# Kernel tuning notes

Measured on AMD Instinct MI355X. Metric: run time of the kernel, lower is better.

Reference implementation:

```python
import jax, jax.numpy as jnp
import numpy as np

MARGIN = 1.0
N, D, NUM_CLASSES = 8192, 512, 64


def setup_inputs() -> dict:
    key = jax.random.key(0)
    kz, kl = jax.random.split(key)
    z = jax.random.normal(kz, (N, D), dtype=jnp.float32)
    labels = jax.random.randint(kl, (N,), 0, NUM_CLASSES, dtype=jnp.int64)
    return {"z": z, "labels": labels}


def _pairwise_dist(z):
    # ||zi - zj|| via gram trick; zero-safe sqrt (grad 0 at zero distance, like torch.cdist)
    sq = jnp.sum(z * z, axis=1)  # [N]
    d2 = jnp.maximum(sq[:, None] + sq[None, :] - 2.0 * (z @ z.T), 0.0)  # [N, N]
    safe = d2 > 0
    return jnp.where(safe, jnp.sqrt(jnp.where(safe, d2, 1.0)), 0.0)


def reference(z, labels):
    n = z.shape[0]
    dist = _pairwise_dist(z)                       # [N, N]
    same = labels[:, None] == labels[None, :]      # [N, N] bool (includes self)
    pos_cnt = jnp.sum(same, axis=1)                # [N] >= 1 (self)
    neg_cnt = n - pos_cnt
    pos_mean = jnp.sum(jnp.where(same, dist, 0.0), axis=1) / jnp.maximum(pos_cnt, 1)
    neg_mean = jnp.sum(jnp.where(same, 0.0, dist), axis=1) / jnp.maximum(neg_cnt, 1)
    valid = (pos_cnt > 1) & (neg_cnt > 0)
    per_row = jax.nn.relu(pos_mean - neg_mean + MARGIN)
    total = jnp.sum(jnp.where(valid, per_row, 0.0))
    count = jnp.sum(valid)
    return total / jnp.maximum(count, 1)
```

## Files before the change

kernel.cpp:

```cpp
#include <hip/hip_runtime.h>
#include <hip/hip_bf16.h>
#include <hip/hip_fp8.h>
#include <stdint.h>

#define NROW 8192
#define DIM  512
#define BM   128
#define BN   128
#define BKB  128
#define NTK  (DIM / BKB)
#define NT   (NROW / BM)
#define NBLK (NT * (NT + 1) / 2)

typedef float f32x4 __attribute__((ext_vector_type(4)));
typedef int   i32x4 __attribute__((ext_vector_type(4)));
typedef int   i32x8 __attribute__((ext_vector_type(8)));

__device__ __forceinline__ float fast_sqrtf(float x) {
    return __builtin_amdgcn_sqrtf(x);
}

__device__ __forceinline__ unsigned char f32_to_e4m3(float f) {
    __hip_fp8_e4m3 q(f);
    return (unsigned char)q.__x;
}

__global__ __launch_bounds__(256) void prep_kernel(
    const float* __restrict__ z, const int* __restrict__ labels,
    unsigned char* __restrict__ zq, float* __restrict__ sq,
    int* __restrict__ hist, float* __restrict__ totals,
    int* __restrict__ done_ctr)
{
    if (blockIdx.x == NROW / 4) {
        __shared__ int lh[64];
        const int tid = threadIdx.x;
        if (tid < 64) lh[tid] = 0;
        __syncthreads();
        for (int i = tid; i < NROW; i += 256)
            atomicAdd(&lh[labels[i]], 1);
        __syncthreads();
        if (tid < 64) hist[tid] = lh[tid];
        if (tid == 64) { totals[0] = 0.f; totals[1] = 0.f; }
        if (tid == 65) { *done_ctr = 0; }
        return;
    }

    const int lane = threadIdx.x & 63;
    const int wave = threadIdx.x >> 6;
    const int row  = blockIdx.x * 4 + wave;

    const float4* zr = (const float4*)(z + (size_t)row * DIM);
    float4 v0 = zr[lane * 2 + 0];
    float4 v1 = zr[lane * 2 + 1];
    float s = v0.x*v0.x + v0.y*v0.y + v0.z*v0.z + v0.w*v0.w
            + v1.x*v1.x + v1.y*v1.y + v1.z*v1.z + v1.w*v1.w;

    union { unsigned char b[8]; int2 v; } pk;
    pk.b[0] = f32_to_e4m3(v0.x); pk.b[1] = f32_to_e4m3(v0.y);
    pk.b[2] = f32_to_e4m3(v0.z); pk.b[3] = f32_to_e4m3(v0.w);
    pk.b[4] = f32_to_e4m3(v1.x); pk.b[5] = f32_to_e4m3(v1.y);
    pk.b[6] = f32_to_e4m3(v1.z); pk.b[7] = f32_to_e4m3(v1.w);
    ((int2*)(zq + (size_t)row * DIM))[lane] = pk.v;

    #pragma unroll
    for (int sft = 1; sft < 64; sft <<= 1) s += __shfl_xor(s, sft);
    if (lane == 0) sq[row] = s;
}

__global__ __launch_bounds__(256, 3) void tile_kernel(
    const unsigned char* __restrict__ zq,
    const float* __restrict__ sq, const int* __restrict__ labels,
    float* __restrict__ partial_pos, float* __restrict__ partial_neg)
{
    __shared__ unsigned char As[BM * BKB];
    __shared__ unsigned char Bs[BN * BKB];

    const int tid  = threadIdx.x;
    const int lane = tid & 63;
    const int wave = tid >> 6;
    const int wm = wave >> 1;
    const int wn = wave & 1;

    const int bid  = (int)blockIdx.x;
    int bidx = (bid & 7) * (NBLK / 8) + (bid >> 3);
    int tm = 0, rem = bidx;
    while (rem >= NT - tm) { rem -= NT - tm; ++tm; }
    const int tn = tm + rem;
    const int row0 = tm * BM;
    const int col0 = tn * BN;
    const bool offdiag = (tm != tn);

    f32x4 acc[4][4];
    #pragma unroll
    for (int m = 0; m < 4; ++m)
        #pragma unroll
        for (int n = 0; n < 4; ++n)
            acc[m][n] = (f32x4){0.f, 0.f, 0.f, 0.f};

    const int srow   = tid >> 3;
    const int sinner = (tid & 7) << 4;
    const int kbsw   = sinner ^ ((srow & 7) << 4);
    const unsigned char* baseA = zq + (size_t)(row0 + srow) * DIM + kbsw;
    const unsigned char* baseB = zq + (size_t)(col0 + srow) * DIM + kbsw;

    const int swz  = (lane & 7) << 4;
    const int hi32 = (lane >> 4) << 5;
    const unsigned char* apc0 = As + (wm * 64 + (lane & 15)) * BKB + ((hi32 +  0) ^ swz);
    const unsigned char* apc1 = As + (wm * 64 + (lane & 15)) * BKB + ((hi32 + 16) ^ swz);
    const unsigned char* bpc0 = Bs + (wn * 64 + (lane & 15)) * BKB + ((hi32 +  0) ^ swz);
    const unsigned char* bpc1 = Bs + (wn * 64 + (lane & 15)) * BKB + ((hi32 + 16) ^ swz);

#define FRAG(pc0, pc1, off)                                                    \
    __builtin_shufflevector(*(const i32x4*)((pc0) + (off)),                    \
                            *(const i32x4*)((pc1) + (off)), 0, 1, 2, 3, 4, 5, 6, 7)

#define MFMA128(a, b, c)                                                       \
    __builtin_amdgcn_mfma_scale_f32_16x16x128_f8f6f4(                          \
        (a), (b), (c), 0, 0, 0, 0x7F7F7F7F, 0, 0x7F7F7F7F)

    #pragma unroll 1
    for (int t = 0; t < NTK; ++t) {
        const int k0 = t * BKB;
        #pragma unroll
        for (int r = 0; r < 4; ++r) {
            __builtin_amdgcn_global_load_lds(
                (const __attribute__((address_space(1))) void*)(baseA + (size_t)r * 32 * DIM + k0),
                (__attribute__((address_space(3))) void*)(As + r * 4096 + tid * 16),
                16, 0, 0);
            __builtin_amdgcn_global_load_lds(
                (const __attribute__((address_space(1))) void*)(baseB + (size_t)r * 32 * DIM + k0),
                (__attribute__((address_space(3))) void*)(Bs + r * 4096 + tid * 16),
                16, 0, 0);
        }
        __syncthreads();

        i32x8 bg0 = FRAG(bpc0, bpc1, 0 * 2048);
        i32x8 bg1 = FRAG(bpc0, bpc1, 1 * 2048);
        i32x8 bg2 = FRAG(bpc0, bpc1, 2 * 2048);
        i32x8 bg3 = FRAG(bpc0, bpc1, 3 * 2048);
        #pragma unroll
        for (int m = 0; m < 4; ++m) {
            i32x8 af = FRAG(apc0, apc1, m * 2048);
            acc[m][0] = MFMA128(af, bg0, acc[m][0]);
            acc[m][1] = MFMA128(af, bg1, acc[m][1]);
            acc[m][2] = MFMA128(af, bg2, acc[m][2]);
            acc[m][3] = MFMA128(af, bg3, acc[m][3]);
        }
        __syncthreads();
    }
#undef FRAG
#undef MFMA128

    const int colbase = col0 + wn * 64;
    const int hi = lane >> 4;
    float csq[4]; int clb[4];
    #pragma unroll
    for (int n = 0; n < 4; ++n) {
        int cg = colbase + n * 16 + (lane & 15);
        csq[n] = sq[cg];
        clb[n] = labels[cg];
    }
    float cpos[4] = {0.f, 0.f, 0.f, 0.f};
    float cneg[4] = {0.f, 0.f, 0.f, 0.f};

    float* rp = (float*)As;
    float* rn = rp + 256;
    float* cp = rp + 512;
    float* cn = rp + 768;

    #pragma unroll
    for (int m = 0; m < 4; ++m) {
        #pragma unroll
        for (int r = 0; r < 4; ++r) {
            const int rowl = wm * 64 + m * 16 + hi * 4 + r;
            const int rg = row0 + rowl;
            const float rs = sq[rg];
            const int   rl = labels[rg];
            float pos = 0.f, neg = 0.f;
            #pragma unroll
            for (int n = 0; n < 4; ++n) {
                float d2   = rs + csq[n] - 2.0f * acc[m][n][r];
                float dist = d2 > 0.f ? fast_sqrtf(d2) : 0.f;
                int cg = colbase + n * 16 + (lane & 15);
                if (cg == rg) dist = 0.f;
                bool same = (rl == clb[n]);
                float dp = same ? dist : 0.f;
                float dn = same ? 0.f : dist;
                pos += dp;  neg += dn;
                cpos[n] += dp;  cneg[n] += dn;
            }
            #pragma unroll
            for (int s = 1; s < 16; s <<= 1) {
                pos += __shfl_xor(pos, s);
                neg += __shfl_xor(neg, s);
            }
            if ((lane & 15) == 0) {
                rp[wn * 128 + rowl] = pos;
                rn[wn * 128 + rowl] = neg;
            }
        }
    }

    #pragma unroll
    for (int n = 0; n < 4; ++n) {
        cpos[n] += __shfl_xor(cpos[n], 16);
        cpos[n] += __shfl_xor(cpos[n], 32);
        cneg[n] += __shfl_xor(cneg[n], 16);
        cneg[n] += __shfl_xor(cneg[n], 32);
        if (lane < 16) {
            int coll = wn * 64 + n * 16 + lane;
            cp[wm * 128 + coll] = cpos[n];
            cn[wm * 128 + coll] = cneg[n];
        }
    }
    __syncthreads();

    if (tid < 128) {
        float p  = rp[tid] + rp[128 + tid];
        float nn = rn[tid] + rn[128 + tid];
        partial_pos[(size_t)tn * NROW + row0 + tid] = p;
        partial_neg[(size_t)tn * NROW + row0 + tid] = nn;
        if (offdiag) {
            float p2 = cp[tid] + cp[128 + tid];
            float n2 = cn[tid] + cn[128 + tid];
            partial_pos[(size_t)tm * NROW + col0 + tid] = p2;
            partial_neg[(size_t)tm * NROW + col0 + tid] = n2;
        }
    }
}

__global__ __launch_bounds__(256) void rowloss_kernel(
    const float* __restrict__ partial_pos, const float* __restrict__ partial_neg,
    const int* __restrict__ labels, const int* __restrict__ hist,
    float* __restrict__ totals, int* __restrict__ done_ctr,
    float* __restrict__ out)
{
    const int i = blockIdx.x * 256 + threadIdx.x;
    float ps = 0.f, ns = 0.f;
    #pragma unroll 8
    for (int s = 0; s < NT; ++s) {
        ps += partial_pos[(size_t)s * NROW + i];
        ns += partial_neg[(size_t)s * NROW + i];
    }
    const float pc = (float)hist[labels[i]];
    const float nc = (float)NROW - pc;
    const float pm = ps / fmaxf(pc, 1.f);
    const float nm = ns / fmaxf(nc, 1.f);
    const bool valid = (pc > 1.f) && (nc > 0.f);
    float t = valid ? fmaxf(pm - nm + 1.0f, 0.f) : 0.f;
    float c = valid ? 1.f : 0.f;
    #pragma unroll
    for (int s = 1; s < 64; s <<= 1) {
        t += __shfl_xor(t, s);
        c += __shfl_xor(c, s);
    }
    __shared__ float blk[8];
    const int wv = threadIdx.x >> 6;
    if ((threadIdx.x & 63) == 0) { blk[wv] = t; blk[4 + wv] = c; }
    __syncthreads();
    if (threadIdx.x == 0) {
        atomicAdd(&totals[0], blk[0] + blk[1] + blk[2] + blk[3]);
        atomicAdd(&totals[1], blk[4] + blk[5] + blk[6] + blk[7]);
        __threadfence();
        int prev = atomicAdd(done_ctr, 1);
        if (prev == (int)gridDim.x - 1) {
            float tt = atomicAdd(&totals[0], 0.f);
            float cc = atomicAdd(&totals[1], 0.f);
            out[0] = tt / fmaxf(cc, 1.f);
        }
    }
}

extern "C" void kernel_launch(void* const* d_in, const int* in_sizes, int n_in,
                              void* d_out, int out_size, void* d_ws, size_t ws_size,
                              hipStream_t stream) {
    (void)in_sizes; (void)n_in; (void)out_size; (void)ws_size;
    const float* z      = (const float*)d_in[0];
    const int*   labels = (const int*)d_in[1];
    float*       out    = (float*)d_out;

    char* ws = (char*)d_ws;
    float* partial_pos = (float*)(ws);
    float* partial_neg = (float*)(ws + 2097152);
    int*   hist     = (int*)  (ws + 4194304);
    float* totals   = (float*)(ws + 4194560);
    int*   done_ctr = (int*)  (ws + 4194568);
    unsigned char* zq = (unsigned char*)(ws + 4194816);
    float* sq       = (float*)(ws + 4194816 + (size_t)NROW * DIM);

    prep_kernel    <<<NROW / 4 + 1, 256, 0, stream>>>(z, labels, zq, sq, hist,
                                                      totals, done_ctr);
    tile_kernel    <<<NBLK, 256, 0, stream>>>(zq, sq, labels, partial_pos, partial_neg);
    rowloss_kernel <<<NROW / 256, 256, 0, stream>>>(partial_pos, partial_neg, labels,
                                                    hist, totals, done_ctr, out);
}
```

Baseline: 65.06 us.

## Double-buffer LDS tiles and split tile kernel across eight waves

The tile kernel now uses 512 threads, so each of eight waves computes a 32x64 sub-tile instead of 64x64. LDS is double-buffered so the next K-slice's global-to-LDS loads are issued before the current slice's MFMAs, leaving one barrier per iteration. The column-partial reduction in the epilogue now sums four wave-row contributions. Shared memory per block doubles to 64KB, which limits how many blocks fit on a CU. With only four K iterations, the overlap has little room to pay off.

After: 152.8 us. +134.8%, slower.

```diff
diff --git a/kernel.cpp b/kernel.cpp
--- a/kernel.cpp
+++ b/kernel.cpp
@@ -67,13 +67,13 @@
     if (lane == 0) sq[row] = s;
 }
 
-__global__ __launch_bounds__(256, 3) void tile_kernel(
+__global__ __launch_bounds__(512, 4) void tile_kernel(
     const unsigned char* __restrict__ zq,
     const float* __restrict__ sq, const int* __restrict__ labels,
     float* __restrict__ partial_pos, float* __restrict__ partial_neg)
 {
-    __shared__ unsigned char As[BM * BKB];
-    __shared__ unsigned char Bs[BN * BKB];
+    __shared__ unsigned char As[2 * BM * BKB];
+    __shared__ unsigned char Bs[2 * BN * BKB];
 
     const int tid  = threadIdx.x;
     const int lane = tid & 63;
@@ -90,9 +90,9 @@
     const int col0 = tn * BN;
     const bool offdiag = (tm != tn);
 
-    f32x4 acc[4][4];
-    #pragma unroll
-    for (int m = 0; m < 4; ++m)
+    f32x4 acc[2][4];
+    #pragma unroll
+    for (int m = 0; m < 2; ++m)
         #pragma unroll
         for (int n = 0; n < 4; ++n)
             acc[m][n] = (f32x4){0.f, 0.f, 0.f, 0.f};
@@ -105,42 +105,44 @@
 
     const int swz  = (lane & 7) << 4;
     const int hi32 = (lane >> 4) << 5;
-    const unsigned char* apc0 = As + (wm * 64 + (lane & 15)) * BKB + ((hi32 +  0) ^ swz);
-    const unsigned char* apc1 = As + (wm * 64 + (lane & 15)) * BKB + ((hi32 + 16) ^ swz);
+    const unsigned char* apc0 = As + (wm * 32 + (lane & 15)) * BKB + ((hi32 +  0) ^ swz);
+    const unsigned char* apc1 = As + (wm * 32 + (lane & 15)) * BKB + ((hi32 + 16) ^ swz);
     const unsigned char* bpc0 = Bs + (wn * 64 + (lane & 15)) * BKB + ((hi32 +  0) ^ swz);
     const unsigned char* bpc1 = Bs + (wn * 64 + (lane & 15)) * BKB + ((hi32 + 16) ^ swz);
 
 #define FRAG(pc0, pc1, off)                                                    \
     __builtin_shufflevector(*(const i32x4*)((pc0) + (off)),                    \
                             *(const i32x4*)((pc1) + (off)), 0, 1, 2, 3, 4, 5, 6, 7)
-
 #define MFMA128(a, b, c)                                                       \
     __builtin_amdgcn_mfma_scale_f32_16x16x128_f8f6f4(                          \
         (a), (b), (c), 0, 0, 0, 0x7F7F7F7F, 0, 0x7F7F7F7F)
-
-    #pragma unroll 1
+#define STAGE(bufofs, k0)                                                      \
+    do {                                                                       \
+        _Pragma("unroll")                                                      \
+        for (int r = 0; r < 2; ++r) {                                          \
+            __builtin_amdgcn_global_load_lds(                                  \
+                (const __attribute__((address_space(1))) void*)(baseA + (size_t)r * 64 * DIM + (k0)), \
+                (__attribute__((address_space(3))) void*)(As + (bufofs) + r * 8192 + tid * 16), 16, 0, 0); \
+            __builtin_amdgcn_global_load_lds(                                  \
+                (const __attribute__((address_space(1))) void*)(baseB + (size_t)r * 64 * DIM + (k0)), \
+                (__attribute__((address_space(3))) void*)(Bs + (bufofs) + r * 8192 + tid * 16), 16, 0, 0); \
+        }                                                                      \
+    } while (0)
+
+    STAGE(0, 0);
+    __syncthreads();
+    #pragma unroll
     for (int t = 0; t < NTK; ++t) {
-        const int k0 = t * BKB;
+        const int cur = (t & 1) * 16384;
+        const int nxt = ((t + 1) & 1) * 16384;
+        if (t + 1 < NTK) STAGE(nxt, (t + 1) * BKB);
+        i32x8 bg0 = FRAG(bpc0 + cur, bpc1 + cur, 0 * 2048);
+        i32x8 bg1 = FRAG(bpc0 + cur, bpc1 + cur, 1 * 2048);
+        i32x8 bg2 = FRAG(bpc0 + cur, bpc1 + cur, 2 * 2048);
+        i32x8 bg3 = FRAG(bpc0 + cur, bpc1 + cur, 3 * 2048);
         #pragma unroll
-        for (int r = 0; r < 4; ++r) {
-            __builtin_amdgcn_global_load_lds(
-                (const __attribute__((address_space(1))) void*)(baseA + (size_t)r * 32 * DIM + k0),
-                (__attribute__((address_space(3))) void*)(As + r * 4096 + tid * 16),
-                16, 0, 0);
-            __builtin_amdgcn_global_load_lds(
-                (const __attribute__((address_space(1))) void*)(baseB + (size_t)r * 32 * DIM + k0),
-                (__attribute__((address_space(3))) void*)(Bs + r * 4096 + tid * 16),
-                16, 0, 0);
-        }
-        __syncthreads();
-
-        i32x8 bg0 = FRAG(bpc0, bpc1, 0 * 2048);
-        i32x8 bg1 = FRAG(bpc0, bpc1, 1 * 2048);
-        i32x8 bg2 = FRAG(bpc0, bpc1, 2 * 2048);
-        i32x8 bg3 = FRAG(bpc0, bpc1, 3 * 2048);
-        #pragma unroll
-        for (int m = 0; m < 4; ++m) {
-            i32x8 af = FRAG(apc0, apc1, m * 2048);
+        for (int m = 0; m < 2; ++m) {
+            i32x8 af = FRAG(apc0 + cur, apc1 + cur, m * 2048);
             acc[m][0] = MFMA128(af, bg0, acc[m][0]);
             acc[m][1] = MFMA128(af, bg1, acc[m][1]);
             acc[m][2] = MFMA128(af, bg2, acc[m][2]);
@@ -150,6 +152,7 @@
     }
 #undef FRAG
 #undef MFMA128
+#undef STAGE
 
     const int colbase = col0 + wn * 64;
     const int hi = lane >> 4;
@@ -166,13 +169,13 @@
     float* rp = (float*)As;
     float* rn = rp + 256;
     float* cp = rp + 512;
-    float* cn = rp + 768;
-
-    #pragma unroll
-    for (int m = 0; m < 4; ++m) {
+    float* cn = rp + 1024;
+
+    #pragma unroll
+    for (int m = 0; m < 2; ++m) {
         #pragma unroll
         for (int r = 0; r < 4; ++r) {
-            const int rowl = wm * 64 + m * 16 + hi * 4 + r;
+            const int rowl = wm * 32 + m * 16 + hi * 4 + r;
             const int rg = row0 + rowl;
             const float rs = sq[rg];
             const int   rl = labels[rg];
@@ -221,8 +224,8 @@
         partial_pos[(size_t)tn * NROW + row0 + tid] = p;
         partial_neg[(size_t)tn * NROW + row0 + tid] = nn;
         if (offdiag) {
-            float p2 = cp[tid] + cp[128 + tid];
-            float n2 = cn[tid] + cn[128 + tid];
+            float p2 = cp[tid] + cp[128 + tid] + cp[256 + tid] + cp[384 + tid];
+            float n2 = cn[tid] + cn[128 + tid] + cn[256 + tid] + cn[384 + tid];
             partial_pos[(size_t)tm * NROW + col0 + tid] = p2;
             partial_neg[(size_t)tm * NROW + col0 + tid] = n2;
         }
@@ -290,7 +293,7 @@
 
     prep_kernel    <<<NROW / 4 + 1, 256, 0, stream>>>(z, labels, zq, sq, hist,
                                                       totals, done_ctr);
-    tile_kernel    <<<NBLK, 256, 0, stream>>>(zq, sq, labels, partial_pos, partial_neg);
+    tile_kernel    <<<NBLK, 512, 0, stream>>>(zq, sq, labels, partial_pos, partial_neg);
     rowloss_kernel <<<NROW / 256, 256, 0, stream>>>(partial_pos, partial_neg, labels,
                                                     hist, totals, done_ctr, out);
 }
```

## Replace row shuffle reductions with LDS transpose and track total instead of negative

Applied to the files above, without the earlier changes.

The epilogue now accumulates pos and total distance and derives neg as total minus pos, which removes a select per element. Per-row partials are written to a padded LDS buffer, and 128 threads then sum them with vector loads, replacing the 16-lane shuffle reductions. The diagonal check is precomputed per lane as a predicate. Shared memory grows to about 42KB, which may reduce occupancy below the three blocks per CU requested by the launch bounds. Computing neg by subtraction can also lose float precision.

Result: faster. 55.42 us, median of 2 (-14.8%).

```diff
diff --git a/kernel.cpp b/kernel.cpp
--- a/kernel.cpp
+++ b/kernel.cpp
@@ -11,6 +11,7 @@
 #define NTK  (DIM / BKB)
 #define NT   (NROW / BM)
 #define NBLK (NT * (NT + 1) / 2)
+#define RST  20
 
 typedef float f32x4 __attribute__((ext_vector_type(4)));
 typedef int   i32x4 __attribute__((ext_vector_type(4)));
@@ -72,8 +73,9 @@
     const float* __restrict__ sq, const int* __restrict__ labels,
     float* __restrict__ partial_pos, float* __restrict__ partial_neg)
 {
-    __shared__ unsigned char As[BM * BKB];
-    __shared__ unsigned char Bs[BN * BKB];
+    __shared__ __align__(16) float smem_f[10752];
+    unsigned char* As = (unsigned char*)smem_f;
+    unsigned char* Bs = (unsigned char*)smem_f + 16384;
 
     const int tid  = threadIdx.x;
     const int lane = tid & 63;
@@ -113,7 +115,6 @@
 #define FRAG(pc0, pc1, off)                                                    \
     __builtin_shufflevector(*(const i32x4*)((pc0) + (off)),                    \
                             *(const i32x4*)((pc1) + (off)), 0, 1, 2, 3, 4, 5, 6, 7)
-
 #define MFMA128(a, b, c)                                                       \
     __builtin_amdgcn_mfma_scale_f32_16x16x128_f8f6f4(                          \
         (a), (b), (c), 0, 0, 0, 0x7F7F7F7F, 0, 0x7F7F7F7F)
@@ -133,7 +134,6 @@
                 16, 0, 0);
         }
         __syncthreads();
-
         i32x8 bg0 = FRAG(bpc0, bpc1, 0 * 2048);
         i32x8 bg1 = FRAG(bpc0, bpc1, 1 * 2048);
         i32x8 bg2 = FRAG(bpc0, bpc1, 2 * 2048);
@@ -151,53 +151,50 @@
 #undef FRAG
 #undef MFMA128
 
+    const int lo = lane & 15;
+    const int hi = lane >> 4;
     const int colbase = col0 + wn * 64;
-    const int hi = lane >> 4;
+
     float csq[4]; int clb[4];
     #pragma unroll
     for (int n = 0; n < 4; ++n) {
-        int cg = colbase + n * 16 + (lane & 15);
+        int cg = colbase + n * 16 + lo;
         csq[n] = sq[cg];
         clb[n] = labels[cg];
     }
+
+    const bool dwv = (!offdiag) && (wm == wn);
+    bool dpred[4];
+    #pragma unroll
+    for (int r = 0; r < 4; ++r)
+        dpred[r] = dwv && (lo == hi * 4 + r);
+
     float cpos[4] = {0.f, 0.f, 0.f, 0.f};
-    float cneg[4] = {0.f, 0.f, 0.f, 0.f};
-
-    float* rp = (float*)As;
-    float* rn = rp + 256;
-    float* cp = rp + 512;
-    float* cn = rp + 768;
+    float ctot[4] = {0.f, 0.f, 0.f, 0.f};
+
+    float* posrow = smem_f + (wn * 128 + wm * 64 + hi * 4) * RST + lo;
+    float* cpb    = smem_f + 10240;
+    float* cnb    = cpb + 256;
 
     #pragma unroll
     for (int m = 0; m < 4; ++m) {
         #pragma unroll
         for (int r = 0; r < 4; ++r) {
-            const int rowl = wm * 64 + m * 16 + hi * 4 + r;
-            const int rg = row0 + rowl;
+            const int rg = row0 + wm * 64 + m * 16 + hi * 4 + r;
             const float rs = sq[rg];
             const int   rl = labels[rg];
-            float pos = 0.f, neg = 0.f;
+            float pos = 0.f, tot = 0.f;
             #pragma unroll
             for (int n = 0; n < 4; ++n) {
                 float d2   = rs + csq[n] - 2.0f * acc[m][n][r];
                 float dist = d2 > 0.f ? fast_sqrtf(d2) : 0.f;
-                int cg = colbase + n * 16 + (lane & 15);
-                if (cg == rg) dist = 0.f;
-                bool same = (rl == clb[n]);
-                float dp = same ? dist : 0.f;
-                float dn = same ? 0.f : dist;
-                pos += dp;  neg += dn;
-                cpos[n] += dp;  cneg[n] += dn;
+                if (n == m) dist = dpred[r] ? 0.f : dist;
+                float dp = (rl == clb[n]) ? dist : 0.f;
+                pos += dp;  tot += dist;
+                cpos[n] += dp;  ctot[n] += dist;
             }
-            #pragma unroll
-            for (int s = 1; s < 16; s <<= 1) {
-                pos += __shfl_xor(pos, s);
-                neg += __shfl_xor(neg, s);
-            }
-            if ((lane & 15) == 0) {
-                rp[wn * 128 + rowl] = pos;
-                rn[wn * 128 + rowl] = neg;
-            }
+            posrow[(m * 16 + r) * RST]        = pos;
+            posrow[(m * 16 + r) * RST + 5120] = tot;
         }
     }
 
@@ -205,26 +202,36 @@
     for (int n = 0; n < 4; ++n) {
         cpos[n] += __shfl_xor(cpos[n], 16);
         cpos[n] += __shfl_xor(cpos[n], 32);
-        cneg[n] += __shfl_xor(cneg[n], 16);
-        cneg[n] += __shfl_xor(cneg[n], 32);
+        ctot[n] += __shfl_xor(ctot[n], 16);
+        ctot[n] += __shfl_xor(ctot[n], 32);
         if (lane < 16) {
             int coll = wn * 64 + n * 16 + lane;
-            cp[wm * 128 + coll] = cpos[n];
-            cn[wm * 128 + coll] = cneg[n];
+            cpb[wm * 128 + coll] = cpos[n];
+            cnb[wm * 128 + coll] = ctot[n];
         }
     }
     __syncthreads();
 
     if (tid < 128) {
-        float p  = rp[tid] + rp[128 + tid];
-        float nn = rn[tid] + rn[128 + tid];
-        partial_pos[(size_t)tn * NROW + row0 + tid] = p;
-        partial_neg[(size_t)tn * NROW + row0 + tid] = nn;
+        float ps = 0.f, ts = 0.f;
+        #pragma unroll
+        for (int w = 0; w < 2; ++w) {
+            const float* pr = smem_f + (w * 128 + tid) * RST;
+            #pragma unroll
+            for (int j = 0; j < 16; j += 4) {
+                f32x4 a = *(const f32x4*)(pr + j);
+                f32x4 b = *(const f32x4*)(pr + 5120 + j);
+                ps += a[0] + a[1] + a[2] + a[3];
+                ts += b[0] + b[1] + b[2] + b[3];
+            }
+        }
+        partial_pos[(size_t)tn * NROW + row0 + tid] = ps;
+        partial_neg[(size_t)tn * NROW + row0 + tid] = ts - ps;
         if (offdiag) {
-            float p2 = cp[tid] + cp[128 + tid];
-            float n2 = cn[tid] + cn[128 + tid];
+            float p2 = cpb[tid] + cpb[128 + tid];
+            float t2 = cnb[tid] + cnb[128 + tid];
             partial_pos[(size_t)tm * NROW + col0 + tid] = p2;
-            partial_neg[(size_t)tm * NROW + col0 + tid] = n2;
+            partial_neg[(size_t)tm * NROW + col0 + tid] = t2 - p2;
         }
     }
 }
```
